# Kernel optimization log

Hardware: AMD Instinct MI355X
Metric: run time of the kernel (lower is better)

## Reference

```python
import jax, jax.numpy as jnp
import numpy as np

V, H, T, B = 32000, 1024, 512, 64

def setup_inputs() -> dict:
    key = jax.random.key(0)
    ks = jax.random.split(key, 20)
    tokens = jax.random.randint(ks[0], (T, B), 0, V)
    s_emb = 1.0 / np.sqrt(V)
    s_g = 1.0 / np.sqrt(2 * H)
    d = {
        'tokens': tokens,
        'emb_w': jax.random.uniform(ks[1], (H, V), jnp.float32, -s_emb, s_emb),
        'emb_b': jax.random.uniform(ks[2], (H,), jnp.float32, -s_emb, s_emb),
    }
    i = 3
    for pfx in ('fwd', 'bwd'):
        for g in ('i', 'o', 'f', 'g'):
            d[f'{pfx}_w{g}'] = jax.random.uniform(ks[i], (H, 2 * H), jnp.float32, -s_g, s_g); i += 1
            d[f'{pfx}_b{g}'] = jax.random.uniform(ks[i % 20], (H,), jnp.float32, -s_g, s_g)
    return d

def _run_lstm(xs, wi, bi, wo, bo, wf, bf, wg, bg):
    # xs: [T, B, H]; manual LSTM recurrence via lax.scan
    h0 = jnp.zeros((xs.shape[1], H), xs.dtype)
    c0 = jnp.zeros((xs.shape[1], H), xs.dtype)
    def step(carry, x):
        h, c = carry
        comb = jnp.concatenate([x, h], axis=1)          # [B, 2H]
        ig = jax.nn.sigmoid(comb @ wi.T + bi)
        og = jax.nn.sigmoid(comb @ wo.T + bo)
        fg = jax.nn.sigmoid(comb @ wf.T + bf)
        cg = jnp.tanh(comb @ wg.T + bg)
        c = fg * c + ig * cg
        h = og * jnp.tanh(c)
        return (h, c), (h, c)
    _, (hs, cs) = jax.lax.scan(step, (h0, c0), xs)
    return hs, cs                                       # [T, B, H] each

def reference(tokens, emb_w, emb_b,
              fwd_wi, fwd_bi, fwd_wo, fwd_bo, fwd_wf, fwd_bf, fwd_wg, fwd_bg,
              bwd_wi, bwd_bi, bwd_wo, bwd_bo, bwd_wf, bwd_bf, bwd_wg, bwd_bg):
    # one_hot(tokens) @ emb_w.T + emb_b == emb_w.T[tokens] + emb_b (dropout in eval mode)
    emb = emb_w.T[tokens] + emb_b                        # [T, B, H]
    f_hs, f_cs = _run_lstm(emb, fwd_wi, fwd_bi, fwd_wo, fwd_bo, fwd_wf, fwd_bf, fwd_wg, fwd_bg)
    # backward pass over reversed sequence; outputs kept in reversed-scan order,
    # matching the original's un-realigned list concatenation.
    b_hs, b_cs = _run_lstm(emb[::-1], bwd_wi, bwd_bi, bwd_wo, bwd_bo, bwd_wf, bwd_bf, bwd_wg, bwd_bg)
    hidden_states = jnp.concatenate([f_hs, b_hs], axis=2)   # [T, B, 2H]
    cell_states = jnp.concatenate([f_cs, b_cs], axis=2)     # [T, B, 2H]
    return hidden_states, cell_states
```

## Files before the change

kernel.cpp:

```cpp
#include <hip/hip_runtime.h>
#include <cstdint>
#include <cstddef>

#define V_SZ 32000
#define H_SZ 1024
#define T_SZ 512
#define B_SZ 64

typedef short short8 __attribute__((ext_vector_type(8)));
typedef float f32x4 __attribute__((ext_vector_type(4)));
typedef unsigned long long u64;

__device__ __forceinline__ short f2bf(float f) {
  union { float f; unsigned u; } v; v.f = f;
  unsigned r = (v.u + 0x7fffu + ((v.u >> 16) & 1u)) >> 16;
  return (short)r;
}

__device__ __forceinline__ void cs8(u64* p, u64 v) {
  __hip_atomic_store(p, v, __ATOMIC_RELAXED, __HIP_MEMORY_SCOPE_AGENT);
}

__device__ __forceinline__ float fsig(float x) {
  return __builtin_amdgcn_rcpf(1.f + __builtin_amdgcn_exp2f(x * -1.44269504f));
}
__device__ __forceinline__ float ftanh(float x) {
  return 1.f - 2.f * __builtin_amdgcn_rcpf(1.f + __builtin_amdgcn_exp2f(x * 2.88539008f));
}

__global__ __launch_bounds__(256) void k_embT(const float* __restrict__ emb_w,
                                              const float* __restrict__ emb_b,
                                              short* __restrict__ embT) {
  __shared__ float tile[64][65];
  const int v0 = blockIdx.x * 64, h0 = blockIdx.y * 64;
  const int c = threadIdx.x & 63, rg = threadIdx.x >> 6;
#pragma unroll
  for (int p = 0; p < 16; ++p) {
    int r = rg * 16 + p;
    tile[r][c] = emb_w[(size_t)(h0 + r) * V_SZ + v0 + c];
  }
  __syncthreads();
  const float bias = emb_b[h0 + c];
#pragma unroll
  for (int p = 0; p < 16; ++p) {
    int vr = rg * 16 + p;
    embT[(size_t)(v0 + vr) * H_SZ + h0 + c] = f2bf(tile[c][vr] + bias);
  }
}

__global__ __launch_bounds__(256) void k_cast(const float* __restrict__ s,
                                              short* __restrict__ d, int n) {
  for (int i = blockIdx.x * 256 + threadIdx.x; i < n; i += gridDim.x * 256)
    d[i] = f2bf(s[i]);
}

__global__ __launch_bounds__(256) void k_copy(const float* __restrict__ s,
                                              float* __restrict__ d, int n) {
  for (int i = blockIdx.x * 256 + threadIdx.x; i < n; i += gridDim.x * 256)
    d[i] = s[i];
}

__global__ __launch_bounds__(512, 2) void k_persist(
    const int* __restrict__ tokens, const short* __restrict__ embT,
    const short* __restrict__ Wbf, const float* __restrict__ biasws,
    short* __restrict__ hbf, unsigned* __restrict__ bar,
    float* __restrict__ out) {
  __shared__ float P_lds[8][32][68];
  __shared__ short h_sh[32][16];

  const int tid = threadIdx.x;
  const int lane = tid & 63, w = tid >> 6;
  const int l15 = lane & 15, l4 = lane >> 4;
  const int d = (int)(blockIdx.x >> 7);
  const int bflat = (int)(blockIdx.x & 127);
  const int bg = bflat >> 6;
  const int cg = bflat & 63;
  const int n0 = cg << 4;
  const int r0 = bg * 32 + l15, r1 = r0 + 16;
  const int kw = w * 32 + l4 * 8;

  short8 Bf[8][4];
#pragma unroll
  for (int jj = 0; jj < 8; ++jj) {
    int slab = w + jj * 8;
#pragma unroll
    for (int nt = 0; nt < 4; ++nt) {
      int row64 = nt * 16 + l15;
      size_t grow = (size_t)((d * 4 + (row64 >> 4)) * 1024 + n0 + (row64 & 15));
      Bf[jj][nt] = *(const short8*)(Wbf + grow * 2048 + slab * 32 + l4 * 8);
    }
  }

  const int b32 = tid >> 4, c16 = tid & 15;
  const int gcol = n0 + c16, gbrow = bg * 32 + b32;
  float brg[4];
#pragma unroll
  for (int g4 = 0; g4 < 4; ++g4) brg[g4] = biasws[d * 4096 + g4 * 1024 + gcol];
  float c_reg = 0.f;

  unsigned* const gflags = bar + (d * 2 + bg) * 64;

  const f32x4 fzero = {0.f, 0.f, 0.f, 0.f};
  f32x4 acc[2][4];

  auto X_PHASE = [&](int s) {
    const int td = d ? (T_SZ - 1 - s) : s;
    const short* xb0 = embT + (size_t)tokens[td * B_SZ + r0] * 1024 + kw;
    const short* xb1 = embT + (size_t)tokens[td * B_SZ + r1] * 1024 + kw;
    short8 xf[2][4];
#pragma unroll
    for (int jj = 0; jj < 4; ++jj) {
      xf[0][jj] = *(const short8*)(xb0 + jj * 256);
      xf[1][jj] = *(const short8*)(xb1 + jj * 256);
    }
#pragma unroll
    for (int ms = 0; ms < 2; ++ms)
#pragma unroll
      for (int nt = 0; nt < 4; ++nt) acc[ms][nt] = fzero;
#pragma unroll
    for (int jj = 0; jj < 4; ++jj)
#pragma unroll
      for (int ms = 0; ms < 2; ++ms)
#pragma unroll
        for (int nt = 0; nt < 4; ++nt)
          acc[ms][nt] = __builtin_amdgcn_mfma_f32_16x16x32_bf16(
              xf[ms][jj], Bf[jj][nt], acc[ms][nt], 0, 0, 0);
  };

  X_PHASE(0);

  for (int t = 0; t < T_SZ; ++t) {
    if (t > 0) {
      const short* hsrc = hbf + ((t & 1) * 2 + d) * 65536;
      const short* hb0 = hsrc + r0 * 1024 + kw;
      const short* hb1 = hsrc + r1 * 1024 + kw;
      short8 hf[2][4];
      asm volatile(
          "global_load_dwordx4 %0, %8, off sc0 sc1\n\t"
          "global_load_dwordx4 %1, %8, off offset:512 sc0 sc1\n\t"
          "global_load_dwordx4 %2, %8, off offset:1024 sc0 sc1\n\t"
          "global_load_dwordx4 %3, %8, off offset:1536 sc0 sc1\n\t"
          "global_load_dwordx4 %4, %9, off sc0 sc1\n\t"
          "global_load_dwordx4 %5, %9, off offset:512 sc0 sc1\n\t"
          "global_load_dwordx4 %6, %9, off offset:1024 sc0 sc1\n\t"
          "global_load_dwordx4 %7, %9, off offset:1536 sc0 sc1\n\t"
          "s_waitcnt vmcnt(0)"
          : "=&v"(hf[0][0]), "=&v"(hf[0][1]), "=&v"(hf[0][2]), "=&v"(hf[0][3]),
            "=&v"(hf[1][0]), "=&v"(hf[1][1]), "=&v"(hf[1][2]), "=&v"(hf[1][3])
          : "v"(hb0), "v"(hb1)
          : "memory");
#pragma unroll
      for (int q = 0; q < 4; ++q)
#pragma unroll
        for (int ms = 0; ms < 2; ++ms)
#pragma unroll
          for (int nt = 0; nt < 4; ++nt)
            acc[ms][nt] = __builtin_amdgcn_mfma_f32_16x16x32_bf16(
                hf[ms][q], Bf[4 + q][nt], acc[ms][nt], 0, 0, 0);
    }

#pragma unroll
    for (int ms = 0; ms < 2; ++ms)
#pragma unroll
      for (int nt = 0; nt < 4; ++nt)
#pragma unroll
        for (int i = 0; i < 4; ++i)
          P_lds[w][ms * 16 + l4 * 4 + i][nt * 16 + l15] = acc[ms][nt][i];
    __syncthreads();

    float pr[4];
#pragma unroll
    for (int g4 = 0; g4 < 4; ++g4) {
      float s = brg[g4];
#pragma unroll
      for (int q = 0; q < 8; ++q) s += P_lds[q][b32][g4 * 16 + c16];
      pr[g4] = s;
    }
    float ig = fsig(pr[0]);
    float og = fsig(pr[1]);
    float fg = fsig(pr[2]);
    float cg4 = ftanh(pr[3]);
    c_reg = fg * c_reg + ig * cg4;
    float hnew = og * ftanh(c_reg);

    if (t < T_SZ - 1) {
      short* hdst = hbf + (((t + 1) & 1) * 2 + d) * 65536;
      h_sh[b32][c16] = f2bf(hnew);
      __syncthreads();
      if (tid < 128) {
        int r = tid >> 2, qq = tid & 3;
        cs8((u64*)(hdst + (bg * 32 + r) * 1024 + n0 + qq * 4),
            *(const u64*)&h_sh[r][qq * 4]);
      }
      __syncthreads();
      if (tid == 0)
        __hip_atomic_store(gflags + cg, (unsigned)(t + 1), __ATOMIC_RELAXED,
                           __HIP_MEMORY_SCOPE_AGENT);

      size_t o = (size_t)(t * B_SZ + gbrow) * 2048 + (size_t)d * 1024 + gcol;
      out[o] = hnew;
      out[o + 67108864] = c_reg;
      X_PHASE(t + 1);

      if (w == 0) {
        const unsigned tgt = (unsigned)(t + 1);
        while (true) {
          unsigned v = __hip_atomic_load(gflags + lane, __ATOMIC_RELAXED,
                                         __HIP_MEMORY_SCOPE_AGENT);
          if (__all(v >= tgt)) break;
          __builtin_amdgcn_s_sleep(1);
        }
      }
      __syncthreads();
    } else {
      size_t o = (size_t)(t * B_SZ + gbrow) * 2048 + (size_t)d * 1024 + gcol;
      out[o] = hnew;
      out[o + 67108864] = c_reg;
    }
  }
}

extern "C" void kernel_launch(void* const* d_in, const int* in_sizes, int n_in,
                              void* d_out, int out_size, void* d_ws, size_t ws_size,
                              hipStream_t stream) {
  (void)in_sizes; (void)n_in; (void)out_size; (void)ws_size;
  const int* tokens  = (const int*)d_in[0];
  const float* emb_w = (const float*)d_in[1];
  const float* emb_b = (const float*)d_in[2];

  char* ws = (char*)d_ws;
  short* embT   = (short*)(ws);
  short* Wbf    = (short*)(ws + 65536000);
  float* biasws = (float*)(ws + 99090432);
  short* hbf    = (short*)(ws + 99123200);
  unsigned* bar = (unsigned*)(ws + 99647488);

  (void)hipMemsetAsync(ws + 99647488, 0, 1024, stream);

  k_embT<<<dim3(500, 16), 256, 0, stream>>>(emb_w, emb_b, embT);

  for (int d = 0; d < 2; ++d)
    for (int g = 0; g < 4; ++g) {
      const float* wsrc = (const float*)d_in[3 + d * 8 + g * 2];
      const float* bsrc = (const float*)d_in[4 + d * 8 + g * 2];
      k_cast<<<1024, 256, 0, stream>>>(wsrc, Wbf + (size_t)(d * 4 + g) * 1024 * 2048,
                                       1024 * 2048);
      k_copy<<<4, 256, 0, stream>>>(bsrc, biasws + (d * 4 + g) * 1024, 1024);
    }

  float* outp = (float*)d_out;
  void* kargs[] = {(void*)&tokens, (void*)&embT, (void*)&Wbf, (void*)&biasws,
                   (void*)&hbf, (void*)&bar, (void*)&outp};
  (void)hipLaunchCooperativeKernel((const void*)k_persist, dim3(256), dim3(512), kargs,
                                   0, stream);
}
```

Measured before the change: 3.101 ms.

## Use per-wave flags and shuffle-packed h stores to cut barrier overhead

Each wave now packs its h values to bf16 with lane shuffles and v_cvt_pk_bf16_f32 and stores them directly, removing the LDS staging buffer and two block barriers. Each wave also publishes its own readiness flag. Every wave then polls the specific flags covering the h rows and columns it needs, instead of wave 0 polling per-block flags and then holding a block barrier. The wait moves to just before the h loads, so the X-phase for the next step runs before waiting. The cost is more flag memory (8 KB memset), more polling traffic, and an extra s_waitcnt before each publish.

```diff
diff --git a/kernel.cpp b/kernel.cpp
--- a/kernel.cpp
+++ b/kernel.cpp
@@ -15,6 +15,12 @@
   union { float f; unsigned u; } v; v.f = f;
   unsigned r = (v.u + 0x7fffu + ((v.u >> 16) & 1u)) >> 16;
   return (short)r;
+}
+
+__device__ __forceinline__ unsigned cvtpk(float a, float b) {
+  unsigned r;
+  asm("v_cvt_pk_bf16_f32 %0, %1, %2" : "=v"(r) : "v"(a), "v"(b));
+  return r;
 }
 
 __device__ __forceinline__ void cs8(u64* p, u64 v) {
@@ -66,7 +72,6 @@
     short* __restrict__ hbf, unsigned* __restrict__ bar,
     float* __restrict__ out) {
   __shared__ float P_lds[8][32][68];
-  __shared__ short h_sh[32][16];
 
   const int tid = threadIdx.x;
   const int lane = tid & 63, w = tid >> 6;
@@ -98,7 +103,10 @@
   for (int g4 = 0; g4 < 4; ++g4) brg[g4] = biasws[d * 4096 + g4 * 1024 + gcol];
   float c_reg = 0.f;
 
-  unsigned* const gflags = bar + (d * 2 + bg) * 64;
+  unsigned* const grpf = bar + (d * 2 + bg) * 512;
+  unsigned* const fpub = grpf + cg * 8 + w;
+  unsigned* const fpoll =
+      grpf + ((lane >> 4) * 16 + 2 * w + ((lane >> 3) & 1)) * 8 + (lane & 7);
 
   const f32x4 fzero = {0.f, 0.f, 0.f, 0.f};
   f32x4 acc[2][4];
@@ -131,6 +139,13 @@
 
   for (int t = 0; t < T_SZ; ++t) {
     if (t > 0) {
+      const unsigned tgt = (unsigned)t;
+      while (true) {
+        unsigned v = __hip_atomic_load(fpoll, __ATOMIC_RELAXED,
+                                       __HIP_MEMORY_SCOPE_AGENT);
+        if (__all(v >= tgt)) break;
+        __builtin_amdgcn_s_sleep(1);
+      }
       const short* hsrc = hbf + ((t & 1) * 2 + d) * 65536;
       const short* hb0 = hsrc + r0 * 1024 + kw;
       const short* hb1 = hsrc + r1 * 1024 + kw;
@@ -185,38 +200,25 @@
 
     if (t < T_SZ - 1) {
       short* hdst = hbf + (((t + 1) & 1) * 2 + d) * 65536;
-      h_sh[b32][c16] = f2bf(hnew);
-      __syncthreads();
-      if (tid < 128) {
-        int r = tid >> 2, qq = tid & 3;
-        cs8((u64*)(hdst + (bg * 32 + r) * 1024 + n0 + qq * 4),
-            *(const u64*)&h_sh[r][qq * 4]);
+      float nb = __shfl_down(hnew, 1);
+      unsigned ulo = cvtpk(hnew, nb);
+      unsigned uhi = __shfl_down(ulo, 2);
+      if ((lane & 3) == 0) {
+        u64 pk = ((u64)uhi << 32) | (u64)ulo;
+        cs8((u64*)(hdst + (size_t)gbrow * 1024 + n0 + (lane & 15)), pk);
       }
-      __syncthreads();
-      if (tid == 0)
-        __hip_atomic_store(gflags + cg, (unsigned)(t + 1), __ATOMIC_RELAXED,
+      asm volatile("s_waitcnt vmcnt(0)" ::: "memory");
+      if (lane == 0)
+        __hip_atomic_store(fpub, (unsigned)(t + 1), __ATOMIC_RELAXED,
                            __HIP_MEMORY_SCOPE_AGENT);
-
-      size_t o = (size_t)(t * B_SZ + gbrow) * 2048 + (size_t)d * 1024 + gcol;
-      out[o] = hnew;
-      out[o + 67108864] = c_reg;
-      X_PHASE(t + 1);
-
-      if (w == 0) {
-        const unsigned tgt = (unsigned)(t + 1);
-        while (true) {
-          unsigned v = __hip_atomic_load(gflags + lane, __ATOMIC_RELAXED,
-                                         __HIP_MEMORY_SCOPE_AGENT);
-          if (__all(v >= tgt)) break;
-          __builtin_amdgcn_s_sleep(1);
-        }
-      }
-      __syncthreads();
-    } else {
-      size_t o = (size_t)(t * B_SZ + gbrow) * 2048 + (size_t)d * 1024 + gcol;
-      out[o] = hnew;
-      out[o + 67108864] = c_reg;
-    }
+    }
+
+    size_t o = (size_t)(t * B_SZ + gbrow) * 2048 + (size_t)d * 1024 + gcol;
+    out[o] = hnew;
+    out[o + 67108864] = c_reg;
+
+    __syncthreads();
+    if (t < T_SZ - 1) X_PHASE(t + 1);
   }
 }
 
@@ -235,7 +237,7 @@
   short* hbf    = (short*)(ws + 99123200);
   unsigned* bar = (unsigned*)(ws + 99647488);
 
-  (void)hipMemsetAsync(ws + 99647488, 0, 1024, stream);
+  (void)hipMemsetAsync(ws + 99647488, 0, 8192, stream);
 
   k_embT<<<dim3(500, 16), 256, 0, stream>>>(emb_w, emb_b, embT);
 
```

New measurement: 3.244 ms. 4.6% more time.
